# Kernel tuning notes

Measured on AMD Instinct MI355X. Metric: run time of the kernel, lower is better.

The kernel has to match this reference:

```python
import jax, jax.numpy as jnp
import numpy as np

N_E = 8192      # codebook size
E_DIM = 256     # codebook dim
BETA = 0.25

def setup_inputs() -> dict:
    key = jax.random.key(0)
    k1, k2 = jax.random.split(key)
    z = jax.random.normal(k1, (4, E_DIM, 16, 16, 16), dtype=jnp.float32)
    weight = jax.random.normal(k2, (N_E, E_DIM), dtype=jnp.float32)
    return {"z": z, "weight": weight}

def reference(z, weight):
    # b c d h w -> b d h w c
    z_t = jnp.transpose(z, (0, 2, 3, 4, 1))
    zf = z_t.reshape(-1, E_DIM)                          # [N, e_dim]
    # l2 pairwise distances: |z|^2 + |w|^2 - 2 z.w^T
    d = (jnp.sum(zf * zf, axis=1, keepdims=True)
         + jnp.sum(weight * weight, axis=1)
         - 2.0 * jnp.einsum('bd,nd->bn', zf, weight))    # [N, n_e]
    idx = jnp.argmin(d, axis=1)                          # [N]
    z_q = weight[idx].reshape(z_t.shape)                 # gather lookup
    # perplexity from cluster assignment histogram (avoids dense one-hot)
    counts = jax.ops.segment_sum(jnp.ones_like(idx, dtype=z.dtype), idx,
                                 num_segments=N_E)
    avg_probs = counts / zf.shape[0]
    perplexity = jnp.exp(-jnp.sum(avg_probs * jnp.log(avg_probs + 1e-10)))
    # commitment loss (z_q detached)
    loss = BETA * jnp.mean((jax.lax.stop_gradient(z_q) - z_t) ** 2)
    # straight-through estimator
    z_q_st = z_t + jax.lax.stop_gradient(z_q - z_t)
    out = jnp.transpose(z_q_st, (0, 4, 1, 2, 3))         # b d h w c -> b c d h w
    return out, loss, perplexity, idx
```

## Files before the change

### kernel.cpp

```cpp
#include <hip/hip_runtime.h>
#include <stdint.h>


#define M_TOTAL 16384
#define N_CODES 8192
#define KDIM    256
#define SPATIAL 4096
#define NSPLIT  8
#define CODES_PER_SPLIT  1024
#define CHUNK_CODES      16
#define CHUNKS_PER_SPLIT 64
#define CHUNK_BYTES      9216
#define CHUNK_HALFS      4608
#define M_BLOCK          256

typedef _Float16 v8hf __attribute__((ext_vector_type(8)));
typedef _Float16 v4hf __attribute__((ext_vector_type(4)));
typedef float    v4f  __attribute__((ext_vector_type(4)));

#define WAITCNT_VM3   0x0F73
#define WAITCNT_VM0   0x0F70
#define WAITCNT_LGKM0 0xC07F

__global__ __launch_bounds__(256) void prep_w_kernel(
    const float* __restrict__ w, _Float16* __restrict__ wpk,
    int* __restrict__ counts, double* __restrict__ loss_acc)
{
    const int t = threadIdx.x;
    const int n = blockIdx.x * 4 + (t >> 6);
    const int lane = t & 63;
    v4f v = ((const v4f*)(w + (size_t)n * KDIM))[lane];
    v4hf hv;
    float s = 0.0f;
#pragma unroll
    for (int j = 0; j < 4; j++) {
        float f = v[j];
        s += f * f;
        hv[j] = (_Float16)f;
    }
    const int chunk = n >> 4;
    const int row   = n & 15;
    const int ks = lane >> 3;
    const int qq = (lane >> 1) & 3;
    const int hh = lane & 1;
    size_t off = (size_t)chunk * CHUNK_HALFS + ks * 512 + qq * 128 + row * 8 + hh * 4;
    *(v4hf*)(wpk + off) = hv;
#pragma unroll
    for (int o = 32; o >= 1; o >>= 1) s += __shfl_xor(s, o);
    if (lane == 0) {
        float* hwp = (float*)((char*)wpk + (size_t)chunk * CHUNK_BYTES + 8192);
        hwp[row] = 1024.0f - 0.5f * s;
    }
    const int gi = blockIdx.x * 256 + t;
    if (gi < N_CODES) counts[gi] = 0;
    if (gi == 0) *loss_acc = 0.0;
}

__device__ __forceinline__ void top2max_merge(uint32_t& v1, int& i1, uint32_t& v2, int& i2,
                                              uint32_t o1, int oi1, uint32_t o2, int oi2) {
    bool ob = (o1 > v1) || (o1 == v1 && oi1 < i1);
    uint32_t n1v, n2v; int n1i, n2i;
    if (ob) {
        bool t2 = (v1 > o2) || (v1 == o2 && i1 < oi2);
        n1v = o1; n1i = oi1;
        n2v = t2 ? v1 : o2; n2i = t2 ? i1 : oi2;
    } else {
        bool t2 = (o1 > v2) || (o1 == v2 && oi1 < i2);
        n1v = v1; n1i = i1;
        n2v = t2 ? o1 : v2; n2i = t2 ? oi1 : i2;
    }
    v1 = n1v; i1 = n1i; v2 = n2v; i2 = n2i;
}

__global__ __launch_bounds__(256, 2) void gemm_kernel(
    const float* __restrict__ z,
    const _Float16* __restrict__ wpk,
    int4* __restrict__ candbuf)
{
    __shared__ __align__(16) _Float16 lds[2][CHUNK_HALFS];

    const int bid   = blockIdx.x;
    const int split = bid & 7;
    const int rb    = bid >> 3;
    const int i0    = rb * M_BLOCK;
    const int b     = i0 >> 12;
    const int s0    = i0 & (SPATIAL - 1);
    const int tid   = threadIdx.x;
    const int wid   = tid >> 6;
    const int lane  = tid & 63;
    const int r     = lane & 15;
    const int q     = lane >> 4;

    const char* wsplit = (const char*)wpk + (size_t)split * CHUNKS_PER_SPLIT * CHUNK_BYTES;

    auto stage = [&](int c, int buf) {
        const char* gb = wsplit + (size_t)c * CHUNK_BYTES;
        char* lb = (char*)&lds[buf][0];
#pragma unroll
        for (int j = 0; j < 2; j++) {
            const int o = (wid * 2 + j) * 1024 + lane * 16;
            __builtin_amdgcn_global_load_lds(
                (const __attribute__((address_space(1))) void*)(gb + o),
                (__attribute__((address_space(3))) void*)(lb + o), 16, 0, 0);
        }
        const int oh = 8192 + wid * 256 + lane * 4;
        __builtin_amdgcn_global_load_lds(
            (const __attribute__((address_space(1))) void*)(gb + oh),
            (__attribute__((address_space(3))) void*)(lb + oh), 4, 0, 0);
    };

    stage(0, 0);
    stage(1, 1);

    v8hf a[4][8];
    {
        const float* zb = z + ((size_t)b << 20) + (size_t)(s0 + wid * 64 + r);
#pragma unroll
        for (int mt = 0; mt < 4; mt++) {
#pragma unroll
            for (int ks = 0; ks < 8; ks++) {
                const int kbase = ks * 32 + q * 8;
#pragma unroll
                for (int j = 0; j < 8; j++)
                    a[mt][ks][j] = (_Float16)zb[((size_t)(kbase + j) << 12) + mt * 16];
            }
        }
    }

    uint32_t k1[4][4], k2[4][4];
#pragma unroll
    for (int mt = 0; mt < 4; mt++)
#pragma unroll
    for (int g = 0; g < 4; g++) { k1[mt][g] = 0u; k2[mt][g] = 0u; }

    auto compute = [&](int it, int buf) {
        const char* lb = (const char*)&lds[buf][0];
        const float hwv = *(const float*)(lb + 8192 + r * 4);
        v4f acc[4];
#pragma unroll
        for (int mt = 0; mt < 4; mt++) acc[mt] = (v4f){hwv, hwv, hwv, hwv};

        __builtin_amdgcn_s_setprio(1);
#pragma unroll
        for (int ks = 0; ks < 8; ks++) {
            v8hf bh = *(const v8hf*)(lb + ks * 1024 + lane * 16);
#pragma unroll
            for (int mt = 0; mt < 4; mt++)
                acc[mt] = __builtin_amdgcn_mfma_f32_16x16x32_f16(a[mt][ks], bh, acc[mt], 0, 0, 0);
        }
        __builtin_amdgcn_s_setprio(0);

        const uint32_t tag = (uint32_t)it;
#pragma unroll
        for (int mt = 0; mt < 4; mt++)
#pragma unroll
        for (int g = 0; g < 4; g++) {
            uint32_t key = (__float_as_uint(acc[mt][g]) & 0xFFFFFFC0u) | tag;
            uint32_t o1 = k1[mt][g], o2 = k2[mt][g];
            uint32_t mn = key < o1 ? key : o1;
            k2[mt][g] = o2 > mn ? o2 : mn;
            k1[mt][g] = key > o1 ? key : o1;
        }
    };

    __builtin_amdgcn_s_waitcnt(WAITCNT_VM0);
    __builtin_amdgcn_s_barrier();

#pragma unroll 2
    for (int it = 0; it < CHUNKS_PER_SPLIT - 2; it++) {
        const int buf = it & 1;
        __builtin_amdgcn_s_waitcnt(WAITCNT_VM3);
        __builtin_amdgcn_s_barrier();
        compute(it, buf);
        __builtin_amdgcn_s_waitcnt(WAITCNT_LGKM0);
        __builtin_amdgcn_s_barrier();
        stage(it + 2, buf);
    }
    __builtin_amdgcn_s_waitcnt(WAITCNT_VM3);
    __builtin_amdgcn_s_barrier();
    compute(CHUNKS_PER_SPLIT - 2, 0);
    __builtin_amdgcn_s_waitcnt(WAITCNT_VM0);
    __builtin_amdgcn_s_barrier();
    compute(CHUNKS_PER_SPLIT - 1, 1);

    const int nsbase = split * CODES_PER_SPLIT + r;
#pragma unroll
    for (int mt = 0; mt < 4; mt++) {
#pragma unroll
        for (int g = 0; g < 4; g++) {
            uint32_t K1 = k1[mt][g], K2 = k2[mt][g];
            int n1 = nsbase + (int)((K1 & 63u) << 4);
            int n2 = nsbase + (int)((K2 & 63u) << 4);
#pragma unroll
            for (int off = 1; off < 16; off <<= 1) {
                uint32_t o1 = __shfl_xor(K1, off);
                int     on1 = __shfl_xor(n1, off);
                uint32_t o2 = __shfl_xor(K2, off);
                int     on2 = __shfl_xor(n2, off);
                top2max_merge(K1, n1, K2, n2, o1, on1, o2, on2);
            }
            if (r == 0) {
                const int row = i0 + wid * 64 + mt * 16 + q * 4 + g;
                candbuf[(size_t)row * 8 + split] = make_int4((int)K1, n1, (int)K2, n2);
            }
        }
    }
}

__global__ __launch_bounds__(256) void finish_kernel(
    const float* __restrict__ z, const float* __restrict__ weight,
    const int4* __restrict__ candbuf,
    int* __restrict__ counts, double* __restrict__ loss_acc,
    float* __restrict__ out, float* __restrict__ out_idx_f)
{
    __shared__ int4  s_cand[32][8];
    __shared__ float s_zw[32][KDIM + 1];
    __shared__ int   s_fi[32];
    __shared__ double s_loss[4];

    const int i0 = blockIdx.x * 32;
    const int b  = i0 >> 12;
    const int s0 = i0 & (SPATIAL - 1);
    const int t  = threadIdx.x;

    s_cand[t >> 3][t & 7] = candbuf[(size_t)(i0 + (t >> 3)) * 8 + (t & 7)];

    for (int e = t; e < 32 * KDIM; e += 256) {
        const int c = e >> 5, rr = e & 31;
        s_zw[rr][c] = z[((size_t)b << 20) + ((size_t)c << 12) + s0 + rr];
    }
    __syncthreads();

    const int row = t >> 3, seg = t & 7;
    float zs[32];
#pragma unroll
    for (int j = 0; j < 32; j++) zs[j] = s_zw[row][seg * 32 + j];

    float da[16];
    float dmin_a = 3.4e38f;
#pragma unroll
    for (int sp = 0; sp < 8; sp++) {
        int4 c = s_cand[row][sp];
        da[sp * 2]     = 2048.0f - 2.0f * __uint_as_float((uint32_t)c.x & 0xFFFFFFC0u);
        da[sp * 2 + 1] = 2048.0f - 2.0f * __uint_as_float((uint32_t)c.z & 0xFFFFFFC0u);
        dmin_a = fminf(dmin_a, fminf(da[sp * 2], da[sp * 2 + 1]));
    }
    const float cutoff = dmin_a + 0.5f;

    double dbest = 1e300; int nbest = 0x7fffffff;
#pragma unroll 1
    for (int c = 0; c < 16; c++) {
        if (da[c] > cutoff) continue;
        int4 cc = s_cand[row][c >> 1];
        const int n = (c & 1) ? cc.w : cc.y;
        const float* wr = weight + (size_t)n * KDIM + seg * 32;
        double d = 0.0;
#pragma unroll
        for (int j = 0; j < 32; j++) {
            double df = (double)zs[j] - (double)wr[j];
            d += df * df;
        }
#pragma unroll
        for (int o = 1; o < 8; o <<= 1) d += __shfl_xor(d, o);
        if (d < dbest || (d == dbest && n < nbest)) { dbest = d; nbest = n; }
    }

    double lsum = 0.0;
    if (seg == 0) {
        s_fi[row] = nbest;
        out_idx_f[i0 + row] = (float)nbest;
        atomicAdd(&counts[nbest], 1);
        lsum = dbest;
    }
#pragma unroll
    for (int o = 1; o < 64; o <<= 1) lsum += __shfl_xor(lsum, o);
    if ((t & 63) == 0) s_loss[t >> 6] = lsum;
    __syncthreads();
    if (t == 0) atomicAdd(loss_acc, s_loss[0] + s_loss[1] + s_loss[2] + s_loss[3]);

    for (int e = t; e < 32 * KDIM; e += 256) {
        const int rr = e >> 8, c = e & 255;
        s_zw[rr][c] = weight[(size_t)s_fi[rr] * KDIM + c];
    }
    __syncthreads();
    const int m = t & 31, c0 = t >> 5;
    const size_t obase = ((size_t)b << 20) + (size_t)(s0 + m);
    for (int c = c0; c < KDIM; c += 8)
        out[obase + ((size_t)c << 12)] = s_zw[m][c];
}

__global__ void finalize_kernel(const int* __restrict__ counts,
                                const double* __restrict__ loss_acc,
                                float* __restrict__ out_scalars)
{
    const int t = threadIdx.x;
    double s = 0.0;
    for (int n = t; n < N_CODES; n += 256) {
        double p = (double)counts[n] / (double)M_TOTAL;
        s -= p * log(p + 1e-10);
    }
#pragma unroll
    for (int o = 32; o >= 1; o >>= 1) s += __shfl_xor(s, o);
    __shared__ double sds[4];
    if ((t & 63) == 0) sds[t >> 6] = s;
    __syncthreads();
    if (t == 0) {
        double tot = sds[0] + sds[1] + sds[2] + sds[3];
        out_scalars[0] = (float)(0.25 * (*loss_acc) / (double)(M_TOTAL * KDIM));
        out_scalars[1] = (float)exp(tot);
    }
}

extern "C" void kernel_launch(void* const* d_in, const int* in_sizes, int n_in,
                              void* d_out, int out_size, void* d_ws, size_t ws_size,
                              hipStream_t stream) {
    const float* z      = (const float*)d_in[0];
    const float* weight = (const float*)d_in[1];
    float* out = (float*)d_out;

    size_t off = 0;
    auto carve = [&](size_t bytes) {
        void* p = (char*)d_ws + off;
        off += (bytes + 255) & ~(size_t)255;
        return p;
    };
    _Float16* wpk     = (_Float16*)carve((size_t)(N_CODES / CHUNK_CODES) * CHUNK_BYTES);
    int4*     candbuf = (int4*)    carve((size_t)M_TOTAL * 8 * 16);
    int*      counts  = (int*)     carve((size_t)N_CODES * 4);
    double*   lossac  = (double*)  carve(16);

    float* out_scalars = out + (size_t)4 * KDIM * SPATIAL;
    float* out_idx_f   = out_scalars + 2;

    prep_w_kernel<<<dim3(N_CODES / 4), dim3(256), 0, stream>>>(weight, wpk, counts, lossac);
    gemm_kernel<<<dim3(M_TOTAL / M_BLOCK * NSPLIT), dim3(256), 0, stream>>>(z, wpk, candbuf);
    finish_kernel<<<dim3(M_TOTAL / 32), dim3(256), 0, stream>>>(
        z, weight, candbuf, counts, lossac, out, out_idx_f);
    finalize_kernel<<<dim3(1), dim3(256), 0, stream>>>(counts, lossac, out_scalars);
}
```

Measured before the change: 192.0 us.

## Pre-pack z to fp16 MFMA layout and triple-buffer codebook staging

```diff
diff --git a/kernel.cpp b/kernel.cpp
--- a/kernel.cpp
+++ b/kernel.cpp
@@ -20,40 +20,56 @@
 
 #define WAITCNT_VM3   0x0F73
 #define WAITCNT_VM0   0x0F70
-#define WAITCNT_LGKM0 0xC07F
-
-__global__ __launch_bounds__(256) void prep_w_kernel(
-    const float* __restrict__ w, _Float16* __restrict__ wpk,
+
+__global__ __launch_bounds__(256) void prep_kernel(
+    const float* __restrict__ w, const float* __restrict__ z,
+    _Float16* __restrict__ wpk, _Float16* __restrict__ z_pk,
     int* __restrict__ counts, double* __restrict__ loss_acc)
 {
     const int t = threadIdx.x;
-    const int n = blockIdx.x * 4 + (t >> 6);
     const int lane = t & 63;
-    v4f v = ((const v4f*)(w + (size_t)n * KDIM))[lane];
-    v4hf hv;
-    float s = 0.0f;
-#pragma unroll
-    for (int j = 0; j < 4; j++) {
-        float f = v[j];
-        s += f * f;
-        hv[j] = (_Float16)f;
-    }
-    const int chunk = n >> 4;
-    const int row   = n & 15;
-    const int ks = lane >> 3;
-    const int qq = (lane >> 1) & 3;
-    const int hh = lane & 1;
-    size_t off = (size_t)chunk * CHUNK_HALFS + ks * 512 + qq * 128 + row * 8 + hh * 4;
-    *(v4hf*)(wpk + off) = hv;
-#pragma unroll
-    for (int o = 32; o >= 1; o >>= 1) s += __shfl_xor(s, o);
-    if (lane == 0) {
-        float* hwp = (float*)((char*)wpk + (size_t)chunk * CHUNK_BYTES + 8192);
-        hwp[row] = 1024.0f - 0.5f * s;
-    }
-    const int gi = blockIdx.x * 256 + t;
-    if (gi < N_CODES) counts[gi] = 0;
-    if (gi == 0) *loss_acc = 0.0;
+    if (blockIdx.x < 2048) {
+        const int n = blockIdx.x * 4 + (t >> 6);
+        v4f v = ((const v4f*)(w + (size_t)n * KDIM))[lane];
+        v4hf hv;
+        float s = 0.0f;
+#pragma unroll
+        for (int j = 0; j < 4; j++) {
+            float f = v[j];
+            s += f * f;
+            hv[j] = (_Float16)f;
+        }
+        const int chunk = n >> 4;
+        const int row   = n & 15;
+        const int ks = lane >> 3;
+        const int qq = (lane >> 1) & 3;
+        const int hh = lane & 1;
+        size_t off = (size_t)chunk * CHUNK_HALFS + ks * 512 + qq * 128 + row * 8 + hh * 4;
+        *(v4hf*)(wpk + off) = hv;
+#pragma unroll
+        for (int o = 32; o >= 1; o >>= 1) s += __shfl_xor(s, o);
+        if (lane == 0) {
+            float* hwp = (float*)((char*)wpk + (size_t)chunk * CHUNK_BYTES + 8192);
+            hwp[row] = 1024.0f - 0.5f * s;
+        }
+        const int gi = blockIdx.x * 256 + t;
+        if (gi < N_CODES) counts[gi] = 0;
+        if (gi == 0) *loss_acc = 0.0;
+    } else {
+        const int zi = blockIdx.x - 2048;
+        const int gw = zi * 4 + (t >> 6);
+        const int g  = gw >> 3;
+        const int ks = gw & 7;
+        const int q  = lane >> 4, r = lane & 15;
+        const int row0 = g << 4;
+        const size_t src = ((size_t)(row0 >> 12) << 20) + (size_t)((row0 & 4095) + r);
+        const int k0 = ks * 32 + q * 8;
+        v8hf hv;
+#pragma unroll
+        for (int j = 0; j < 8; j++)
+            hv[j] = (_Float16)z[src + ((size_t)(k0 + j) << 12)];
+        *(v8hf*)(z_pk + (size_t)g * 4096 + ks * 512 + q * 128 + r * 8) = hv;
+    }
 }
 
 __device__ __forceinline__ void top2max_merge(uint32_t& v1, int& i1, uint32_t& v2, int& i2,
@@ -73,18 +89,16 @@
 }
 
 __global__ __launch_bounds__(256, 2) void gemm_kernel(
-    const float* __restrict__ z,
+    const _Float16* __restrict__ z_pk,
     const _Float16* __restrict__ wpk,
     int4* __restrict__ candbuf)
 {
-    __shared__ __align__(16) _Float16 lds[2][CHUNK_HALFS];
+    __shared__ __align__(16) _Float16 lds[3][CHUNK_HALFS];
 
     const int bid   = blockIdx.x;
     const int split = bid & 7;
     const int rb    = bid >> 3;
     const int i0    = rb * M_BLOCK;
-    const int b     = i0 >> 12;
-    const int s0    = i0 & (SPATIAL - 1);
     const int tid   = threadIdx.x;
     const int wid   = tid >> 6;
     const int lane  = tid & 63;
@@ -93,9 +107,9 @@
 
     const char* wsplit = (const char*)wpk + (size_t)split * CHUNKS_PER_SPLIT * CHUNK_BYTES;
 
-    auto stage = [&](int c, int buf) {
+    auto stage = [&](int c, _Float16* lbh) {
         const char* gb = wsplit + (size_t)c * CHUNK_BYTES;
-        char* lb = (char*)&lds[buf][0];
+        char* lb = (char*)lbh;
 #pragma unroll
         for (int j = 0; j < 2; j++) {
             const int o = (wid * 2 + j) * 1024 + lane * 16;
@@ -109,22 +123,17 @@
             (__attribute__((address_space(3))) void*)(lb + oh), 4, 0, 0);
     };
 
-    stage(0, 0);
-    stage(1, 1);
+    stage(0, lds[0]);
+    stage(1, lds[1]);
 
     v8hf a[4][8];
     {
-        const float* zb = z + ((size_t)b << 20) + (size_t)(s0 + wid * 64 + r);
-#pragma unroll
-        for (int mt = 0; mt < 4; mt++) {
-#pragma unroll
-            for (int ks = 0; ks < 8; ks++) {
-                const int kbase = ks * 32 + q * 8;
-#pragma unroll
-                for (int j = 0; j < 8; j++)
-                    a[mt][ks][j] = (_Float16)zb[((size_t)(kbase + j) << 12) + mt * 16];
-            }
-        }
+        const int g0 = (i0 + wid * 64) >> 4;
+#pragma unroll
+        for (int mt = 0; mt < 4; mt++)
+#pragma unroll
+        for (int ks = 0; ks < 8; ks++)
+            a[mt][ks] = *(const v8hf*)(z_pk + (size_t)(g0 + mt) * 4096 + ks * 512 + q * 128 + r * 8);
     }
 
     uint32_t k1[4][4], k2[4][4];
@@ -133,8 +142,8 @@
 #pragma unroll
     for (int g = 0; g < 4; g++) { k1[mt][g] = 0u; k2[mt][g] = 0u; }
 
-    auto compute = [&](int it, int buf) {
-        const char* lb = (const char*)&lds[buf][0];
+    auto compute = [&](int it, const _Float16* lbh) {
+        const char* lb = (const char*)lbh;
         const float hwv = *(const float*)(lb + 8192 + r * 4);
         v4f acc[4];
 #pragma unroll
@@ -163,25 +172,25 @@
         }
     };
 
+    const _Float16 *pA = lds[0], *pB = lds[1];
+    _Float16 *pC = lds[2];
+#pragma unroll 1
+    for (int it = 0; it < CHUNKS_PER_SPLIT - 2; it++) {
+        __builtin_amdgcn_s_waitcnt(WAITCNT_VM3);
+        __builtin_amdgcn_s_barrier();
+        __builtin_amdgcn_sched_barrier(0);
+        compute(it, pA);
+        stage(it + 2, pC);
+        const _Float16* tmp = pA; pA = pB; pB = pC; pC = (_Float16*)tmp;
+    }
+    __builtin_amdgcn_s_waitcnt(WAITCNT_VM3);
+    __builtin_amdgcn_s_barrier();
+    __builtin_amdgcn_sched_barrier(0);
+    compute(CHUNKS_PER_SPLIT - 2, pA);
     __builtin_amdgcn_s_waitcnt(WAITCNT_VM0);
     __builtin_amdgcn_s_barrier();
-
-#pragma unroll 2
-    for (int it = 0; it < CHUNKS_PER_SPLIT - 2; it++) {
-        const int buf = it & 1;
-        __builtin_amdgcn_s_waitcnt(WAITCNT_VM3);
-        __builtin_amdgcn_s_barrier();
-        compute(it, buf);
-        __builtin_amdgcn_s_waitcnt(WAITCNT_LGKM0);
-        __builtin_amdgcn_s_barrier();
-        stage(it + 2, buf);
-    }
-    __builtin_amdgcn_s_waitcnt(WAITCNT_VM3);
-    __builtin_amdgcn_s_barrier();
-    compute(CHUNKS_PER_SPLIT - 2, 0);
-    __builtin_amdgcn_s_waitcnt(WAITCNT_VM0);
-    __builtin_amdgcn_s_barrier();
-    compute(CHUNKS_PER_SPLIT - 1, 1);
+    __builtin_amdgcn_sched_barrier(0);
+    compute(CHUNKS_PER_SPLIT - 1, pB);
 
     const int nsbase = split * CODES_PER_SPLIT + r;
 #pragma unroll
@@ -253,12 +262,16 @@
         if (da[c] > cutoff) continue;
         int4 cc = s_cand[row][c >> 1];
         const int n = (c & 1) ? cc.w : cc.y;
-        const float* wr = weight + (size_t)n * KDIM + seg * 32;
+        const v4f* wr = (const v4f*)(weight + (size_t)n * KDIM + seg * 32);
         double d = 0.0;
 #pragma unroll
-        for (int j = 0; j < 32; j++) {
-            double df = (double)zs[j] - (double)wr[j];
-            d += df * df;
+        for (int jj = 0; jj < 8; jj++) {
+            v4f wv = wr[jj];
+#pragma unroll
+            for (int u = 0; u < 4; u++) {
+                double df = (double)zs[jj * 4 + u] - (double)wv[u];
+                d += df * df;
+            }
         }
 #pragma unroll
         for (int o = 1; o < 8; o <<= 1) d += __shfl_xor(d, o);
@@ -325,6 +338,7 @@
         return p;
     };
     _Float16* wpk     = (_Float16*)carve((size_t)(N_CODES / CHUNK_CODES) * CHUNK_BYTES);
+    _Float16* z_pk    = (_Float16*)carve((size_t)M_TOTAL * KDIM * 2);
     int4*     candbuf = (int4*)    carve((size_t)M_TOTAL * 8 * 16);
     int*      counts  = (int*)     carve((size_t)N_CODES * 4);
     double*   lossac  = (double*)  carve(16);
@@ -332,8 +346,8 @@
     float* out_scalars = out + (size_t)4 * KDIM * SPATIAL;
     float* out_idx_f   = out_scalars + 2;
 
-    prep_w_kernel<<<dim3(N_CODES / 4), dim3(256), 0, stream>>>(weight, wpk, counts, lossac);
-    gemm_kernel<<<dim3(M_TOTAL / M_BLOCK * NSPLIT), dim3(256), 0, stream>>>(z, wpk, candbuf);
+    prep_kernel<<<dim3(4096), dim3(256), 0, stream>>>(weight, z, wpk, z_pk, counts, lossac);
+    gemm_kernel<<<dim3(M_TOTAL / M_BLOCK * NSPLIT), dim3(256), 0, stream>>>(z_pk, wpk, candbuf);
     finish_kernel<<<dim3(M_TOTAL / 32), dim3(256), 0, stream>>>(
         z, weight, candbuf, counts, lossac, out, out_idx_f);
     finalize_kernel<<<dim3(1), dim3(256), 0, stream>>>(counts, lossac, out_scalars);
```

Result: faster. 183.8 us (-4.3%).
